# Kernel tuning notes

Measured on AMD Instinct MI355X. Metric: run time of the kernel, lower is better.

## Reference

```python
import jax, jax.numpy as jnp
import numpy as np

B = 512            # number of graphs in the batch
P = 256            # nodes per graph (== max_graph_size, graphs are equal-sized)
N = B * P          # total nodes
E = 2 * 1024 * 1024
F = 64             # node_feat_size
LAYERS = [32, 32, 32, 1]


def setup_inputs() -> dict:
    key = jax.random.key(0)
    ks = jax.random.split(key, 16)
    x = jax.random.normal(ks[0], (N, F), dtype=jnp.float32)
    edge_index = jax.random.randint(ks[1], (2, E), 0, N, dtype=jnp.int32)
    batch = (jnp.arange(N, dtype=jnp.int32) // P)   # sorted graph ids, equal sizes
    edge_mask = jax.random.uniform(ks[2], (E,), dtype=jnp.float32)
    # layer weights (DGCNN layer: out = D^-1 @ A_tilde @ X @ W + b)
    dims = [F] + LAYERS
    params = {}
    for i in range(len(LAYERS)):
        fan = dims[i]
        params[f"W{i}"] = jax.random.normal(ks[3 + 2 * i], (dims[i], dims[i + 1]), dtype=jnp.float32) / np.sqrt(fan)
        params[f"b{i}"] = jnp.zeros((dims[i + 1],), dtype=jnp.float32)
    return {"x": x, "edge_index": edge_index, "batch": batch, "edge_mask": edge_mask, **params}


def _build_matrices(x, edge_index, batch, edge_mask):
    # counts / exclusive starts per graph (batch is sorted)
    ones = jnp.ones_like(batch)
    counts = jax.ops.segment_sum(ones, batch, num_segments=B)
    starts = jnp.cumsum(counts) - counts                       # [B]
    src, dst = edge_index[0], edge_index[1]
    g = batch[src]
    valid = (batch[src] == batch[dst])                          # drop cross-graph edges
    ls = jnp.clip(src - starts[g], 0, P - 1)
    ld = jnp.clip(dst - starts[g], 0, P - 1)
    w = jnp.where(valid, edge_mask, 0.0)
    # padded A_tilde = A + I  (duplicate edges accumulate, as sparse COO add does)
    adj = jnp.zeros((B, P, P), dtype=x.dtype).at[g, ls, ld].add(w)
    adj = adj + jnp.eye(P, dtype=x.dtype)[None]
    # reciprocal degree of A_tilde, nan/inf -> 0
    deg = adj.sum(axis=2)                                       # [B, P]
    rinv = jnp.where(deg > 0, 1.0 / deg, 0.0)
    feats = x.reshape(B, P, F)                                  # equal-size graphs -> trivial pad
    return adj, rinv, feats


def reference(x, edge_index, batch, edge_mask, W0, b0, W1, b1, W2, b2, W3, b3):
    adj, rinv, h = _build_matrices(x, edge_index, batch, edge_mask)
    for W, b in ((W0, b0), (W1, b1), (W2, b2), (W3, b3)):
        h = jnp.einsum('bnm,bmf->bnf', adj, h @ W)              # A_tilde @ X @ W
        h = rinv[..., None] * h + b                             # D^-1 scaling + bias
        h = jnp.tanh(h)
    return h
```

## Files before the change

### kernel.cpp

```cpp
#include <hip/hip_runtime.h>
#include <hip/hip_bf16.h>

#define BGR 512
#define PP  256
#define NN  (BGR * PP)
#define EE  (2 * 1024 * 1024)
#define RCAP 4


__global__ void k_escatter(const int* __restrict__ ei, const float* __restrict__ emask,
                           int* __restrict__ rowcnt, int2* __restrict__ ebkt) {
    int e0 = (blockIdx.x * 256 + threadIdx.x) * 4;
    int4 s4 = *reinterpret_cast<const int4*>(ei + e0);
    int4 d4 = *reinterpret_cast<const int4*>(ei + EE + e0);
#pragma unroll
    for (int j = 0; j < 4; j++) {
        int s = (&s4.x)[j];
        int d = (&d4.x)[j];
        if ((s >> 8) != (d >> 8)) continue;
        float w = emask[e0 + j];
        int pos = atomicAdd(&rowcnt[s], 1);
        if (pos < RCAP) ebkt[s * RCAP + pos] = make_int2(d & 255, __float_as_int(w));
    }
}

__device__ __forceinline__ float fast_tanh(float x) {
    float t = __expf(2.0f * x);
    return 1.0f - __fdividef(2.0f, 1.0f + t);
}

template <int KH>
__device__ __forceinline__ void pmv32(const float (&h)[KH], const float* __restrict__ W,
                                      float (&P)[32]) {
#pragma unroll
    for (int c = 0; c < 32; c++) P[c] = 0.f;
#pragma unroll
    for (int k = 0; k < KH; k++) {
        const float hk = h[k];
#pragma unroll
        for (int c = 0; c < 32; c++) P[c] += hk * W[k * 32 + c];
    }
}


__global__ __launch_bounds__(512, 2)
void k_fused(const float* __restrict__ x,
             const float* __restrict__ W0, const float* __restrict__ b0,
             const float* __restrict__ W1, const float* __restrict__ b1,
             const float* __restrict__ W2, const float* __restrict__ b2,
             const float* __restrict__ W3, const float* __restrict__ b3,
             const int* __restrict__ rowcnt, const int2* __restrict__ ebkt,
             float* __restrict__ out) {
    __shared__ float Psl[2][PP][36];

    const int t    = threadIdx.x;
    const int g    = blockIdx.x;
    const int row  = t & 255;
    const int half = __builtin_amdgcn_readfirstlane(t >> 8);
    const int cb   = half * 16;

    const int node = g * PP + row;

    const int cnt = min(rowcnt[node], RCAP);
    int   eld[RCAP];
    float ewt[RCAP];
    float wsum = 0.f;
#pragma unroll
    for (int j = 0; j < RCAP; j++) {
        if (j < cnt) {
            int2 v = ebkt[node * RCAP + j];
            eld[j] = v.x;
            ewt[j] = __int_as_float(v.y);
            wsum += ewt[j];
        } else {
            eld[j] = row;
            ewt[j] = 0.f;
        }
    }
    const float rv = 1.0f / (1.0f + wsum);

    float xr[32];
    const float* xrow = x + (size_t)node * 64 + half * 32;
#pragma unroll
    for (int k = 0; k < 32; k += 4) {
        float4 v = *reinterpret_cast<const float4*>(xrow + k);
        xr[k] = v.x; xr[k + 1] = v.y; xr[k + 2] = v.z; xr[k + 3] = v.w;
    }

    float P[32];
    float acc[16];
    float h[16];

    const float* Ws0 = W0 + half * (32 * 32);
    const float* Ws1 = W1 + half * (16 * 32);
    const float* Ws2 = W2 + half * (16 * 32);

    float (*own)[36]       = Psl[half];
    const float (*par)[36] = Psl[1 - half];
    const float (*sA)[36]  = Psl[0];
    const float (*sB)[36]  = Psl[1];

#pragma unroll
    for (int L = 0; L < 3; L++) {
        if (L == 0)      pmv32<32>(xr, Ws0, P);
        else if (L == 1) pmv32<16>(h, Ws1, P);
        else             pmv32<16>(h, Ws2, P);

#pragma unroll
        for (int j = 0; j < 32; j += 4)
            *reinterpret_cast<float4*>(&own[row][j]) =
                make_float4(P[j], P[j + 1], P[j + 2], P[j + 3]);
        __syncthreads();

#pragma unroll
        for (int j = 0; j < 16; j += 4) {
            float4 q = *reinterpret_cast<const float4*>(&par[row][cb + j]);
            acc[j]     = P[cb + j]     + q.x;
            acc[j + 1] = P[cb + j + 1] + q.y;
            acc[j + 2] = P[cb + j + 2] + q.z;
            acc[j + 3] = P[cb + j + 3] + q.w;
        }

#pragma unroll
        for (int e = 0; e < RCAP; e++) {
            if (ewt[e] != 0.f) {
                int ld = eld[e];
                float w = ewt[e];
#pragma unroll
                for (int j = 0; j < 16; j += 4) {
                    float4 ya = *reinterpret_cast<const float4*>(&sA[ld][cb + j]);
                    float4 yb = *reinterpret_cast<const float4*>(&sB[ld][cb + j]);
                    acc[j]     += w * (ya.x + yb.x);
                    acc[j + 1] += w * (ya.y + yb.y);
                    acc[j + 2] += w * (ya.z + yb.z);
                    acc[j + 3] += w * (ya.w + yb.w);
                }
            }
        }

        const float* b = (L == 0) ? b0 : (L == 1) ? b1 : b2;
#pragma unroll
        for (int j = 0; j < 16; j++) h[j] = fast_tanh(rv * acc[j] + b[cb + j]);
        __syncthreads();
    }

    float a = 0.f;
#pragma unroll
    for (int k = 0; k < 16; k++) a += h[k] * W3[cb + k];
    Psl[0][row][32 + half] = a;
    __syncthreads();
    if (half == 0) {
        float z = Psl[0][row][32] + Psl[0][row][33];
#pragma unroll
        for (int e = 0; e < RCAP; e++) {
            if (ewt[e] != 0.f) {
                int ld = eld[e];
                z += ewt[e] * (Psl[0][ld][32] + Psl[0][ld][33]);
            }
        }
        out[node] = fast_tanh(rv * z + b3[0]);
    }
}


extern "C" void kernel_launch(void* const* d_in, const int* in_sizes, int n_in,
                              void* d_out, int out_size, void* d_ws, size_t ws_size,
                              hipStream_t stream) {
    const float* x     = (const float*)d_in[0];
    const int*   ei    = (const int*)d_in[1];
    const float* emask = (const float*)d_in[3];
    const float* W0 = (const float*)d_in[4];
    const float* b0 = (const float*)d_in[5];
    const float* W1 = (const float*)d_in[6];
    const float* b1 = (const float*)d_in[7];
    const float* W2 = (const float*)d_in[8];
    const float* b2 = (const float*)d_in[9];
    const float* W3 = (const float*)d_in[10];
    const float* b3 = (const float*)d_in[11];
    float* out = (float*)d_out;

    int*  rowcnt = (int*)d_ws;
    int2* ebkt   = (int2*)(rowcnt + NN);

    hipMemsetAsync(d_ws, 0, (size_t)NN * sizeof(int), stream);

    k_escatter<<<EE / 1024, 256, 0, stream>>>(ei, emask, rowcnt, ebkt);

    k_fused<<<BGR, 512, 0, stream>>>(x, W0, b0, W1, b1, W2, b2, W3, b3,
                                     rowcnt, ebkt, out);
}
```

Before: 129.8 us.

## Fuse edge scatter into main kernel using a software grid barrier

The separate edge-bucketing kernel is merged into the fused GNN kernel. Each of the 512 blocks first scatters 4096 edges into per-row buckets, then waits at an atomic-counter grid barrier before running the layers. This removes one kernel launch and its launch gap. In exchange all blocks must be co-resident, otherwise the barrier deadlocks, and the spin-wait puts a serialization point between the two phases.

```diff
diff --git a/kernel.cpp b/kernel.cpp
--- a/kernel.cpp
+++ b/kernel.cpp
@@ -8,32 +8,14 @@
 #define RCAP 4
 
 
-__global__ void k_escatter(const int* __restrict__ ei, const float* __restrict__ emask,
-                           int* __restrict__ rowcnt, int2* __restrict__ ebkt) {
-    int e0 = (blockIdx.x * 256 + threadIdx.x) * 4;
-    int4 s4 = *reinterpret_cast<const int4*>(ei + e0);
-    int4 d4 = *reinterpret_cast<const int4*>(ei + EE + e0);
-#pragma unroll
-    for (int j = 0; j < 4; j++) {
-        int s = (&s4.x)[j];
-        int d = (&d4.x)[j];
-        if ((s >> 8) != (d >> 8)) continue;
-        float w = emask[e0 + j];
-        int pos = atomicAdd(&rowcnt[s], 1);
-        if (pos < RCAP) ebkt[s * RCAP + pos] = make_int2(d & 255, __float_as_int(w));
-    }
-}
-
 __device__ __forceinline__ float fast_tanh(float x) {
     float t = __expf(2.0f * x);
     return 1.0f - __fdividef(2.0f, 1.0f + t);
 }
 
 template <int KH>
-__device__ __forceinline__ void pmv32(const float (&h)[KH], const float* __restrict__ W,
-                                      float (&P)[32]) {
-#pragma unroll
-    for (int c = 0; c < 32; c++) P[c] = 0.f;
+__device__ __forceinline__ void pmv_acc(const float (&h)[KH], const float* __restrict__ W,
+                                        float (&P)[32]) {
 #pragma unroll
     for (int k = 0; k < KH; k++) {
         const float hk = h[k];
@@ -42,23 +24,56 @@
     }
 }
 
+__device__ __forceinline__ void grid_barrier(int* ctr) {
+    __syncthreads();
+    if (threadIdx.x == 0) {
+        __threadfence();
+        __hip_atomic_fetch_add(ctr, 1, __ATOMIC_ACQ_REL, __HIP_MEMORY_SCOPE_AGENT);
+        while (__hip_atomic_load(ctr, __ATOMIC_ACQUIRE, __HIP_MEMORY_SCOPE_AGENT) < BGR)
+            __builtin_amdgcn_s_sleep(2);
+        __threadfence();
+    }
+    __syncthreads();
+}
+
 
 __global__ __launch_bounds__(512, 2)
-void k_fused(const float* __restrict__ x,
-             const float* __restrict__ W0, const float* __restrict__ b0,
-             const float* __restrict__ W1, const float* __restrict__ b1,
-             const float* __restrict__ W2, const float* __restrict__ b2,
-             const float* __restrict__ W3, const float* __restrict__ b3,
-             const int* __restrict__ rowcnt, const int2* __restrict__ ebkt,
-             float* __restrict__ out) {
+void k_all(const float* __restrict__ x, const int* __restrict__ ei,
+           const float* __restrict__ emask,
+           const float* __restrict__ W0, const float* __restrict__ b0,
+           const float* __restrict__ W1, const float* __restrict__ b1,
+           const float* __restrict__ W2, const float* __restrict__ b2,
+           const float* __restrict__ W3, const float* __restrict__ b3,
+           int* __restrict__ bar, int* __restrict__ rowcnt,
+           int2* __restrict__ ebkt, float* __restrict__ out) {
     __shared__ float Psl[2][PP][36];
 
-    const int t    = threadIdx.x;
-    const int g    = blockIdx.x;
+    const int t  = threadIdx.x;
+    const int g  = blockIdx.x;
+    const int gt = g * 512 + t;
+
+    {
+        const int e0 = gt * 8;
+#pragma unroll
+        for (int hh = 0; hh < 2; hh++) {
+            int4 s4 = *reinterpret_cast<const int4*>(ei + e0 + hh * 4);
+            int4 d4 = *reinterpret_cast<const int4*>(ei + EE + e0 + hh * 4);
+#pragma unroll
+            for (int j = 0; j < 4; j++) {
+                int s = (&s4.x)[j];
+                int d = (&d4.x)[j];
+                if ((s >> 8) != (d >> 8)) continue;
+                float w = emask[e0 + hh * 4 + j];
+                int pos = atomicAdd(&rowcnt[s], 1);
+                if (pos < RCAP) ebkt[s * RCAP + pos] = make_int2(d & 255, __float_as_int(w));
+            }
+        }
+    }
+    grid_barrier(bar);
+
     const int row  = t & 255;
     const int half = __builtin_amdgcn_readfirstlane(t >> 8);
     const int cb   = half * 16;
-
     const int node = g * PP + row;
 
     const int cnt = min(rowcnt[node], RCAP);
@@ -102,9 +117,11 @@
 
 #pragma unroll
     for (int L = 0; L < 3; L++) {
-        if (L == 0)      pmv32<32>(xr, Ws0, P);
-        else if (L == 1) pmv32<16>(h, Ws1, P);
-        else             pmv32<16>(h, Ws2, P);
+#pragma unroll
+        for (int c = 0; c < 32; c++) P[c] = 0.f;
+        if (L == 0)      pmv_acc<32>(xr, Ws0, P);
+        else if (L == 1) pmv_acc<16>(h, Ws1, P);
+        else             pmv_acc<16>(h, Ws2, P);
 
 #pragma unroll
         for (int j = 0; j < 32; j += 4)
@@ -155,7 +172,7 @@
         for (int e = 0; e < RCAP; e++) {
             if (ewt[e] != 0.f) {
                 int ld = eld[e];
-                z += ewt[e] * (Psl[0][ld][32] + Psl[0][ld][33]);
+                z += ewt[e] * (Psl[0][ld][32] + Psl[0][ld][34 - 1]);
             }
         }
         out[node] = fast_tanh(rv * z + b3[0]);
@@ -179,13 +196,13 @@
     const float* b3 = (const float*)d_in[11];
     float* out = (float*)d_out;
 
-    int*  rowcnt = (int*)d_ws;
+    int*  bar    = (int*)d_ws;
+    int*  rowcnt = bar + 16;
     int2* ebkt   = (int2*)(rowcnt + NN);
 
-    hipMemsetAsync(d_ws, 0, (size_t)NN * sizeof(int), stream);
-
-    k_escatter<<<EE / 1024, 256, 0, stream>>>(ei, emask, rowcnt, ebkt);
-
-    k_fused<<<BGR, 512, 0, stream>>>(x, W0, b0, W1, b1, W2, b2, W3, b3,
-                                     rowcnt, ebkt, out);
-}
+    hipMemsetAsync(d_ws, 0, (size_t)(16 + NN) * sizeof(int), stream);
+
+    void* args_unused = nullptr; (void)args_unused;
+    k_all<<<BGR, 512, 0, stream>>>(x, ei, emask, W0, b0, W1, b1, W2, b2, W3, b3,
+                                   bar, rowcnt, ebkt, out);
+}
```

New measurement: 188.3 us. 45.1% more time.
